# Performance work log

Hardware: AMD Instinct MI355X
Metric: run time of the kernel (lower is better)

Reference implementation:

```python
import jax, jax.numpy as jnp
import numpy as np

N = 100000        # nodes per batch
B = 1             # batch_size
E = 3200000       # edges
IN_F = 128        # in_features
ATT = 128         # attention_dim
HEADS = 8
DK = ATT // HEADS
SLOPE = 0.2       # leaky_relu_slope


def setup_inputs() -> dict:
    key = jax.random.key(0)
    k1, k2, k3, k4 = jax.random.split(key, 4)
    x = jax.random.normal(k1, (B * N, IN_F), dtype=jnp.float32)
    edge = jax.random.randint(k2, (B, 2, E), 0, N)
    # xavier_normal with gain=1.414 on W:[IN_F, ATT]
    W = jax.random.normal(k3, (IN_F, ATT), dtype=jnp.float32) * (1.414 * np.sqrt(2.0 / (IN_F + ATT)))
    # a originally [1, 2*d_k, 1, 1]; flattened to [2*d_k] (same math)
    a = jax.random.normal(k4, (2 * DK,), dtype=jnp.float32) * (1.414 * np.sqrt(2.0 / (2 * DK + 1)))
    return {"x": x, "edge": edge, "W": W, "a": a}


def _segment_softmax(scores, seg):
    # scores: [E, H], seg: [E] -> softmax within each segment (node id)
    smax = jax.ops.segment_max(scores, seg, num_segments=N)
    ex = jnp.exp(scores - smax[seg])
    denom = jax.ops.segment_sum(ex, seg, num_segments=N)
    return ex / denom[seg]


def reference(x, edge, W, a):
    wx = x @ W                                           # [B*N, ATT]
    h = wx.reshape(B, N, HEADS, DK).transpose(0, 1, 3, 2)  # [B, N, DK, H]
    a1, a2 = a[:DK], a[DK:]
    # sum(a * concat(h_src, h_dst)) = a1.h_src + a2.h_dst (linearity)
    s_src = jnp.einsum('bnkh,k->bnh', h, a1)             # [B, N, H]
    s_dst = jnp.einsum('bnkh,k->bnh', h, a2)             # [B, N, H]
    src = edge[:, 0, :]                                  # [B, E]
    dst = edge[:, 1, :]                                  # [B, E]
    gather = jax.vmap(lambda s, i: s[i])
    scores = gather(s_src, src) + gather(s_dst, dst)     # [B, E, H]
    edge_e = jnp.where(scores > 0, scores, SLOPE * scores)  # leaky relu
    # attention_norm_idx = 0 -> normalize over edges sharing a source node
    attention = jax.vmap(_segment_softmax)(edge_e, src)  # [B, E, H]
    return attention, wx
```

## Files before the change

kernel.cpp:

```cpp
#include <hip/hip_runtime.h>

#define N_NODES 100000
#define E_EDGES 3200000
#define IN_F 128
#define ATT 128
#define HEADS 8
#define DK 16
#define SLOPE 0.2f
#define NH (N_NODES * HEADS)

#define CHUNK 448
#define NBINS 224
#define NS 8
#define HB 512
#define EPB 6272

__global__ __launch_bounds__(256) void gemm_s_kernel(
    const float* __restrict__ x, const float* __restrict__ W,
    const float* __restrict__ a, float* __restrict__ wx,
    float* __restrict__ s_src, float* __restrict__ s_dst)
{
    __shared__ float xs[8][128];
    __shared__ float Ws[8][128];

    const int tid = threadIdx.x;
    const int ty  = tid >> 4;
    const int tx  = tid & 15;
    const int row0 = blockIdx.x * 128;

    float acc[8][8];
#pragma unroll
    for (int i = 0; i < 8; i++)
#pragma unroll
        for (int j = 0; j < 8; j++) acc[i][j] = 0.f;

    const int lrow  = tid >> 1;
    const int khalf = (tid & 1) * 4;
    const int wkk   = tid >> 5;
    const int wc    = (tid & 31) * 4;

    for (int k0 = 0; k0 < IN_F; k0 += 8) {
        float4 xv = make_float4(0.f, 0.f, 0.f, 0.f);
        const int grow = row0 + lrow;
        if (grow < N_NODES)
            xv = *(const float4*)(x + (size_t)grow * IN_F + k0 + khalf);
        const float4 wv = *(const float4*)(W + (size_t)(k0 + wkk) * ATT + wc);

        __syncthreads();
        xs[khalf + 0][lrow] = xv.x;
        xs[khalf + 1][lrow] = xv.y;
        xs[khalf + 2][lrow] = xv.z;
        xs[khalf + 3][lrow] = xv.w;
        *(float4*)(&Ws[wkk][wc]) = wv;
        __syncthreads();

#pragma unroll
        for (int kk = 0; kk < 8; kk++) {
            float av[8], bv[8];
            *(float4*)(av)     = *(const float4*)(&xs[kk][ty * 8]);
            *(float4*)(av + 4) = *(const float4*)(&xs[kk][ty * 8 + 4]);
            *(float4*)(bv)     = *(const float4*)(&Ws[kk][tx * 8]);
            *(float4*)(bv + 4) = *(const float4*)(&Ws[kk][tx * 8 + 4]);
#pragma unroll
            for (int r = 0; r < 8; r++)
#pragma unroll
                for (int c = 0; c < 8; c++)
                    acc[r][c] = fmaf(av[r], bv[c], acc[r][c]);
        }
    }

    const int koff = (tx & 1) * 8;
    const int head = tx >> 1;
    float a1[8], a2[8];
#pragma unroll
    for (int c = 0; c < 8; c++) {
        a1[c] = a[koff + c];
        a2[c] = a[DK + koff + c];
    }

#pragma unroll
    for (int r = 0; r < 8; r++) {
        const int grow = row0 + ty * 8 + r;
        const bool ok = (grow < N_NODES);
        if (ok) {
            *(float4*)(wx + (size_t)grow * ATT + tx * 8) =
                make_float4(acc[r][0], acc[r][1], acc[r][2], acc[r][3]);
            *(float4*)(wx + (size_t)grow * ATT + tx * 8 + 4) =
                make_float4(acc[r][4], acc[r][5], acc[r][6], acc[r][7]);
        }
        float p1 = 0.f, p2 = 0.f;
#pragma unroll
        for (int c = 0; c < 8; c++) {
            p1 = fmaf(acc[r][c], a1[c], p1);
            p2 = fmaf(acc[r][c], a2[c], p2);
        }
        p1 += __shfl_xor(p1, 1);
        p2 += __shfl_xor(p2, 1);
        if (((tx & 1) == 0) && ok) {
            s_src[(size_t)grow * HEADS + head] = p1;
            s_dst[(size_t)grow * HEADS + head] = p2;
        }
    }
}

__global__ __launch_bounds__(256) void hist_kernel(
    const int* __restrict__ src, int* __restrict__ counts)
{
    __shared__ int h[NBINS];
    const int t = threadIdx.x;
    const int b = blockIdx.x;
    for (int i = t; i < NBINS; i += 256) h[i] = 0;
    __syncthreads();

    const int rb = b * EPB;
    const int re = min(rb + EPB, E_EDGES);
    for (int i = rb + t * 4; i < re; i += 256 * 4) {
        const int4 s4 = *(const int4*)(src + i);
        atomicAdd(&h[s4.x / CHUNK], 1);
        atomicAdd(&h[s4.y / CHUNK], 1);
        atomicAdd(&h[s4.z / CHUNK], 1);
        atomicAdd(&h[s4.w / CHUNK], 1);
    }
    __syncthreads();
    for (int i = t; i < NBINS; i += 256) counts[i * HB + b] = h[i];
}

__global__ __launch_bounds__(1024) void scan_kernel(
    const int* __restrict__ counts, int* __restrict__ offs)
{
    __shared__ int part[1024];
    const int t = threadIdx.x;
    const int per = (NBINS * HB) / 1024;
    const int base = t * per;

    int sum = 0;
    for (int i = 0; i < per; i++) sum += counts[base + i];
    part[t] = sum;
    __syncthreads();

    for (int off = 1; off < 1024; off <<= 1) {
        int v = 0;
        if (t >= off) v = part[t - off];
        __syncthreads();
        if (t >= off) part[t] += v;
        __syncthreads();
    }

    int run = (t == 0) ? 0 : part[t - 1];
    for (int i = 0; i < per; i++) {
        offs[base + i] = run;
        run += counts[base + i];
    }
}

__global__ __launch_bounds__(256) void scatter_kernel(
    const int* __restrict__ src, const int* __restrict__ dst,
    const int* __restrict__ offs, unsigned int* __restrict__ binned)
{
    __shared__ int cur[NBINS];
    const int t = threadIdx.x;
    const int b = blockIdx.x;
    for (int i = t; i < NBINS; i += 256) cur[i] = offs[i * HB + b];
    __syncthreads();

    const int rb = b * EPB;
    const int re = min(rb + EPB, E_EDGES);
    for (int i = rb + t * 4; i < re; i += 256 * 4) {
        const int4 s4 = *(const int4*)(src + i);
        const int4 d4 = *(const int4*)(dst + i);
        const int ss[4] = {s4.x, s4.y, s4.z, s4.w};
        const int dd[4] = {d4.x, d4.y, d4.z, d4.w};
#pragma unroll
        for (int j = 0; j < 4; j++) {
            const int c = ss[j] / CHUNK;
            const int pos = atomicAdd(&cur[c], 1);
            binned[pos] = ((unsigned int)(ss[j] - c * CHUNK) << 17) |
                          (unsigned int)dd[j];
        }
    }
}

__global__ __launch_bounds__(256, 8) void denom_binned_kernel(
    const unsigned int* __restrict__ binned, const int* __restrict__ offs,
    const float* __restrict__ s_src, const float* __restrict__ s_dst,
    float* __restrict__ denoms)
{
    __shared__ float acc[HEADS][CHUNK + 1];

    const int t  = threadIdx.x;
    const int c  = blockIdx.x;
    const int j  = blockIdx.y;
    const int lo = c * CHUNK;
    const int hi = min(lo + CHUNK, N_NODES);

    for (int i = t; i < HEADS * (CHUNK + 1); i += 256)
        ((float*)acc)[i] = 0.f;
    __syncthreads();

    const int start = offs[c * HB];
    const int end   = (c + 1 < NBINS) ? offs[(c + 1) * HB] : E_EDGES;
    const int len   = end - start;
    const int e0 = start + (int)((long long)len * j / NS);
    const int e1 = start + (int)((long long)len * (j + 1) / NS);

    int i = e0 + t;
    bool v0 = i < e1;
    bool v1 = i + 256 < e1;
    unsigned int pw0 = v0 ? binned[i] : 0u;
    unsigned int pw1 = v1 ? binned[i + 256] : 0u;

    while (v0) {
        const unsigned int w0 = pw0;
        const unsigned int w1 = v1 ? pw1 : pw0;
        const bool cv1 = v1;

        i += 512;
        v0 = i < e1;
        v1 = i + 256 < e1;
        if (v0) pw0 = binned[i];
        if (v1) pw1 = binned[i + 256];

        const int di0 = w0 & 0x1FFFF, sl0 = w0 >> 17;
        const int di1 = w1 & 0x1FFFF, sl1 = w1 >> 17;
        const float4* ps0 = (const float4*)(s_src + (size_t)(lo + sl0) * HEADS);
        const float4* pd0 = (const float4*)(s_dst + (size_t)di0 * HEADS);
        const float4* ps1 = (const float4*)(s_src + (size_t)(lo + sl1) * HEADS);
        const float4* pd1 = (const float4*)(s_dst + (size_t)di1 * HEADS);
        const float4 xa0 = ps0[0], xa1 = ps0[1], xb0 = pd0[0], xb1 = pd0[1];
        const float4 ya0 = ps1[0], ya1 = ps1[1], yb0 = pd1[0], yb1 = pd1[1];
        const float s0[8] = {xa0.x + xb0.x, xa0.y + xb0.y, xa0.z + xb0.z, xa0.w + xb0.w,
                             xa1.x + xb1.x, xa1.y + xb1.y, xa1.z + xb1.z, xa1.w + xb1.w};
        const float s1[8] = {ya0.x + yb0.x, ya0.y + yb0.y, ya0.z + yb0.z, ya0.w + yb0.w,
                             ya1.x + yb1.x, ya1.y + yb1.y, ya1.z + yb1.z, ya1.w + yb1.w};
#pragma unroll
        for (int h = 0; h < 8; h++) {
            float v = s0[h]; v = v > 0.f ? v : SLOPE * v;
            atomicAdd(&acc[h][sl0], __expf(v));
        }
        if (cv1) {
#pragma unroll
            for (int h = 0; h < 8; h++) {
                float v = s1[h]; v = v > 0.f ? v : SLOPE * v;
                atomicAdd(&acc[h][sl1], __expf(v));
            }
        }
    }
    __syncthreads();

    float* outp = denoms + (size_t)j * NH + (size_t)lo * HEADS;
    for (int nd = t; nd < hi - lo; nd += 256) {
        const float4 o0 = make_float4(acc[0][nd], acc[1][nd], acc[2][nd], acc[3][nd]);
        const float4 o1 = make_float4(acc[4][nd], acc[5][nd], acc[6][nd], acc[7][nd]);
        *(float4*)(outp + (size_t)nd * 8)     = o0;
        *(float4*)(outp + (size_t)nd * 8 + 4) = o1;
    }
}

__global__ __launch_bounds__(256) void reduce_recip_kernel(float* __restrict__ denoms)
{
    const int i = blockIdx.x * 256 + threadIdx.x;
    if (i >= NH) return;
    float s = 0.f;
#pragma unroll
    for (int c = 0; c < NS; c++) s += denoms[(size_t)c * NH + i];
    denoms[i] = __frcp_rn(s);
}

__global__ __launch_bounds__(256) void norm_kernel(
    const int* __restrict__ src, const int* __restrict__ dst,
    const float* __restrict__ s_src, const float* __restrict__ s_dst,
    const float* __restrict__ rdenom, float* __restrict__ att)
{
    const int e = blockIdx.x * 256 + threadIdx.x;
    if (e >= E_EDGES) return;
    const int s = src[e];
    const int d = dst[e];
    const float4* ps = (const float4*)(s_src + (size_t)s * HEADS);
    const float4* pd = (const float4*)(s_dst + (size_t)d * HEADS);
    const float4 s0 = ps[0], s1 = ps[1], d0 = pd[0], d1 = pd[1];
    const float4* pr = (const float4*)(rdenom + (size_t)s * HEADS);
    const float4 r0 = pr[0], r1 = pr[1];
    float sc[8] = {s0.x + d0.x, s0.y + d0.y, s0.z + d0.z, s0.w + d0.w,
                   s1.x + d1.x, s1.y + d1.y, s1.z + d1.z, s1.w + d1.w};
    float rd[8] = {r0.x, r0.y, r0.z, r0.w, r1.x, r1.y, r1.z, r1.w};
    float o[8];
#pragma unroll
    for (int h = 0; h < 8; h++) {
        float v = sc[h];
        v = v > 0.f ? v : SLOPE * v;
        o[h] = __expf(v) * rd[h];
    }
    float4* po = (float4*)(att + (size_t)e * HEADS);
    po[0] = make_float4(o[0], o[1], o[2], o[3]);
    po[1] = make_float4(o[4], o[5], o[6], o[7]);
}

extern "C" void kernel_launch(void* const* d_in, const int* in_sizes, int n_in,
                              void* d_out, int out_size, void* d_ws, size_t ws_size,
                              hipStream_t stream)
{
    const float* x    = (const float*)d_in[0];
    const int*   edge = (const int*)d_in[1];
    const float* W    = (const float*)d_in[2];
    const float* a    = (const float*)d_in[3];

    float* out = (float*)d_out;
    float* att = out;
    float* wx  = out + (size_t)E_EDGES * HEADS;

    float* ws     = (float*)d_ws;
    float* s_src  = ws;
    float* s_dst  = s_src + (size_t)NH;
    float* denoms = s_dst + (size_t)NH;
    int*   counts = (int*)(denoms + (size_t)NS * NH);
    int*   offs   = counts + (size_t)NBINS * HB;

    unsigned int* binned = (unsigned int*)att;

    const int* src = edge;
    const int* dst = edge + E_EDGES;

    const int gemm_blocks = (N_NODES + 127) / 128;
    gemm_s_kernel<<<gemm_blocks, 256, 0, stream>>>(x, W, a, wx, s_src, s_dst);

    hist_kernel<<<HB, 256, 0, stream>>>(src, counts);
    scan_kernel<<<1, 1024, 0, stream>>>(counts, offs);
    scatter_kernel<<<HB, 256, 0, stream>>>(src, dst, offs, binned);

    dim3 bgrid(NBINS, NS);
    denom_binned_kernel<<<bgrid, 256, 0, stream>>>(binned, offs, s_src, s_dst, denoms);

    const int nblocks = (NH + 255) / 256;
    reduce_recip_kernel<<<nblocks, 256, 0, stream>>>(denoms);

    const int eblocks = (E_EDGES + 255) / 256;
    norm_kernel<<<eblocks, 256, 0, stream>>>(src, dst, s_src, s_dst, denoms, att);
}
```

Before: 557.1 us.

## Write unnormalized exp scores during binned denom pass, normalize in place

The binned denominator kernel now also carries the original edge index, computes the exp scores once, and scatters them directly into the attention output. The final pass only rescales by the reciprocal denominator, so it no longer gathers s_src and s_dst. The per-slice denominator buffers and the reduce kernel are replaced by global float atomics into one zeroed buffer. The source scores for each chunk are staged in shared memory. In exchange, the binned entries double to 8 bytes and move into workspace, att writes become scattered, the kernel allows fewer blocks per CU (launch bound 5 instead of 8), and denominator summation order is no longer deterministic.

```diff
diff --git a/kernel.cpp b/kernel.cpp
--- a/kernel.cpp
+++ b/kernel.cpp
@@ -103,6 +103,12 @@
     }
 }
 
+__global__ __launch_bounds__(256) void zero_kernel(float4* __restrict__ p)
+{
+    const int i = blockIdx.x * 256 + threadIdx.x;
+    if (i < NH / 4) p[i] = make_float4(0.f, 0.f, 0.f, 0.f);
+}
+
 __global__ __launch_bounds__(256) void hist_kernel(
     const int* __restrict__ src, int* __restrict__ counts)
 {
@@ -155,7 +161,7 @@
 
 __global__ __launch_bounds__(256) void scatter_kernel(
     const int* __restrict__ src, const int* __restrict__ dst,
-    const int* __restrict__ offs, unsigned int* __restrict__ binned)
+    const int* __restrict__ offs, uint2* __restrict__ binned)
 {
     __shared__ int cur[NBINS];
     const int t = threadIdx.x;
@@ -174,18 +180,20 @@
         for (int j = 0; j < 4; j++) {
             const int c = ss[j] / CHUNK;
             const int pos = atomicAdd(&cur[c], 1);
-            binned[pos] = ((unsigned int)(ss[j] - c * CHUNK) << 17) |
-                          (unsigned int)dd[j];
-        }
-    }
-}
-
-__global__ __launch_bounds__(256, 8) void denom_binned_kernel(
-    const unsigned int* __restrict__ binned, const int* __restrict__ offs,
+            binned[pos] = make_uint2(
+                ((unsigned int)(ss[j] - c * CHUNK) << 17) | (unsigned int)dd[j],
+                (unsigned int)(i + j));
+        }
+    }
+}
+
+__global__ __launch_bounds__(256, 5) void denom_binned_kernel(
+    const uint2* __restrict__ binned, const int* __restrict__ offs,
     const float* __restrict__ s_src, const float* __restrict__ s_dst,
-    float* __restrict__ denoms)
+    float* __restrict__ denoms, float* __restrict__ att)
 {
     __shared__ float acc[HEADS][CHUNK + 1];
+    __shared__ float ssrc[CHUNK * HEADS];
 
     const int t  = threadIdx.x;
     const int c  = blockIdx.x;
@@ -195,6 +203,12 @@
 
     for (int i = t; i < HEADS * (CHUNK + 1); i += 256)
         ((float*)acc)[i] = 0.f;
+    {
+        const int nf4 = (hi - lo) * 2;
+        const float4* sp = (const float4*)(s_src + (size_t)lo * HEADS);
+        float4* dp = (float4*)ssrc;
+        for (int i = t; i < nf4; i += 256) dp[i] = sp[i];
+    }
     __syncthreads();
 
     const int start = offs[c * HB];
@@ -206,12 +220,12 @@
     int i = e0 + t;
     bool v0 = i < e1;
     bool v1 = i + 256 < e1;
-    unsigned int pw0 = v0 ? binned[i] : 0u;
-    unsigned int pw1 = v1 ? binned[i + 256] : 0u;
+    uint2 pw0 = v0 ? binned[i] : make_uint2(0u, 0u);
+    uint2 pw1 = v1 ? binned[i + 256] : make_uint2(0u, 0u);
 
     while (v0) {
-        const unsigned int w0 = pw0;
-        const unsigned int w1 = v1 ? pw1 : pw0;
+        const uint2 w0 = pw0;
+        const uint2 w1 = v1 ? pw1 : pw0;
         const bool cv1 = v1;
 
         i += 512;
@@ -220,79 +234,79 @@
         if (v0) pw0 = binned[i];
         if (v1) pw1 = binned[i + 256];
 
-        const int di0 = w0 & 0x1FFFF, sl0 = w0 >> 17;
-        const int di1 = w1 & 0x1FFFF, sl1 = w1 >> 17;
-        const float4* ps0 = (const float4*)(s_src + (size_t)(lo + sl0) * HEADS);
+        const int sl0 = (int)(w0.x >> 17), di0 = (int)(w0.x & 0x1FFFFu);
+        const int sl1 = (int)(w1.x >> 17), di1 = (int)(w1.x & 0x1FFFFu);
+        const int ei0 = (int)w0.y, ei1 = (int)w1.y;
+
         const float4* pd0 = (const float4*)(s_dst + (size_t)di0 * HEADS);
-        const float4* ps1 = (const float4*)(s_src + (size_t)(lo + sl1) * HEADS);
         const float4* pd1 = (const float4*)(s_dst + (size_t)di1 * HEADS);
-        const float4 xa0 = ps0[0], xa1 = ps0[1], xb0 = pd0[0], xb1 = pd0[1];
-        const float4 ya0 = ps1[0], ya1 = ps1[1], yb0 = pd1[0], yb1 = pd1[1];
+        const float4 xb0 = pd0[0], xb1 = pd0[1];
+        const float4 yb0 = pd1[0], yb1 = pd1[1];
+        const float4* qs0 = (const float4*)(ssrc + sl0 * HEADS);
+        const float4* qs1 = (const float4*)(ssrc + sl1 * HEADS);
+        const float4 xa0 = qs0[0], xa1 = qs0[1];
+        const float4 ya0 = qs1[0], ya1 = qs1[1];
+
         const float s0[8] = {xa0.x + xb0.x, xa0.y + xb0.y, xa0.z + xb0.z, xa0.w + xb0.w,
                              xa1.x + xb1.x, xa1.y + xb1.y, xa1.z + xb1.z, xa1.w + xb1.w};
         const float s1[8] = {ya0.x + yb0.x, ya0.y + yb0.y, ya0.z + yb0.z, ya0.w + yb0.w,
                              ya1.x + yb1.x, ya1.y + yb1.y, ya1.z + yb1.z, ya1.w + yb1.w};
+        float ex0[8], ex1[8];
 #pragma unroll
         for (int h = 0; h < 8; h++) {
             float v = s0[h]; v = v > 0.f ? v : SLOPE * v;
-            atomicAdd(&acc[h][sl0], __expf(v));
-        }
+            ex0[h] = __expf(v);
+            float u = s1[h]; u = u > 0.f ? u : SLOPE * u;
+            ex1[h] = __expf(u);
+        }
+        {
+            float4* pa = (float4*)(att + (size_t)ei0 * HEADS);
+            pa[0] = make_float4(ex0[0], ex0[1], ex0[2], ex0[3]);
+            pa[1] = make_float4(ex0[4], ex0[5], ex0[6], ex0[7]);
+        }
+#pragma unroll
+        for (int h = 0; h < 8; h++)
+            atomicAdd(&acc[h][sl0], ex0[h]);
         if (cv1) {
-#pragma unroll
-            for (int h = 0; h < 8; h++) {
-                float v = s1[h]; v = v > 0.f ? v : SLOPE * v;
-                atomicAdd(&acc[h][sl1], __expf(v));
-            }
-        }
-    }
-    __syncthreads();
-
-    float* outp = denoms + (size_t)j * NH + (size_t)lo * HEADS;
+            float4* pa = (float4*)(att + (size_t)ei1 * HEADS);
+            pa[0] = make_float4(ex1[0], ex1[1], ex1[2], ex1[3]);
+            pa[1] = make_float4(ex1[4], ex1[5], ex1[6], ex1[7]);
+#pragma unroll
+            for (int h = 0; h < 8; h++)
+                atomicAdd(&acc[h][sl1], ex1[h]);
+        }
+    }
+    __syncthreads();
+
     for (int nd = t; nd < hi - lo; nd += 256) {
-        const float4 o0 = make_float4(acc[0][nd], acc[1][nd], acc[2][nd], acc[3][nd]);
-        const float4 o1 = make_float4(acc[4][nd], acc[5][nd], acc[6][nd], acc[7][nd]);
-        *(float4*)(outp + (size_t)nd * 8)     = o0;
-        *(float4*)(outp + (size_t)nd * 8 + 4) = o1;
-    }
-}
-
-__global__ __launch_bounds__(256) void reduce_recip_kernel(float* __restrict__ denoms)
-{
-    const int i = blockIdx.x * 256 + threadIdx.x;
-    if (i >= NH) return;
-    float s = 0.f;
-#pragma unroll
-    for (int c = 0; c < NS; c++) s += denoms[(size_t)c * NH + i];
-    denoms[i] = __frcp_rn(s);
+#pragma unroll
+        for (int h = 0; h < 8; h++)
+            unsafeAtomicAdd(&denoms[(size_t)(lo + nd) * HEADS + h], acc[h][nd]);
+    }
 }
 
 __global__ __launch_bounds__(256) void norm_kernel(
-    const int* __restrict__ src, const int* __restrict__ dst,
-    const float* __restrict__ s_src, const float* __restrict__ s_dst,
-    const float* __restrict__ rdenom, float* __restrict__ att)
+    const int* __restrict__ src, const float* __restrict__ denoms,
+    float* __restrict__ att)
 {
     const int e = blockIdx.x * 256 + threadIdx.x;
     if (e >= E_EDGES) return;
+    float4* pa = (float4*)(att + (size_t)e * HEADS);
+    const float4 x0 = pa[0], x1 = pa[1];
     const int s = src[e];
-    const int d = dst[e];
-    const float4* ps = (const float4*)(s_src + (size_t)s * HEADS);
-    const float4* pd = (const float4*)(s_dst + (size_t)d * HEADS);
-    const float4 s0 = ps[0], s1 = ps[1], d0 = pd[0], d1 = pd[1];
-    const float4* pr = (const float4*)(rdenom + (size_t)s * HEADS);
-    const float4 r0 = pr[0], r1 = pr[1];
-    float sc[8] = {s0.x + d0.x, s0.y + d0.y, s0.z + d0.z, s0.w + d0.w,
-                   s1.x + d1.x, s1.y + d1.y, s1.z + d1.z, s1.w + d1.w};
-    float rd[8] = {r0.x, r0.y, r0.z, r0.w, r1.x, r1.y, r1.z, r1.w};
-    float o[8];
-#pragma unroll
-    for (int h = 0; h < 8; h++) {
-        float v = sc[h];
-        v = v > 0.f ? v : SLOPE * v;
-        o[h] = __expf(v) * rd[h];
-    }
-    float4* po = (float4*)(att + (size_t)e * HEADS);
-    po[0] = make_float4(o[0], o[1], o[2], o[3]);
-    po[1] = make_float4(o[4], o[5], o[6], o[7]);
+    const float4* pd = (const float4*)(denoms + (size_t)s * HEADS);
+    const float4 d0 = pd[0], d1 = pd[1];
+    float4 o0, o1;
+    o0.x = x0.x * __frcp_rn(d0.x);
+    o0.y = x0.y * __frcp_rn(d0.y);
+    o0.z = x0.z * __frcp_rn(d0.z);
+    o0.w = x0.w * __frcp_rn(d0.w);
+    o1.x = x1.x * __frcp_rn(d1.x);
+    o1.y = x1.y * __frcp_rn(d1.y);
+    o1.z = x1.z * __frcp_rn(d1.z);
+    o1.w = x1.w * __frcp_rn(d1.w);
+    pa[0] = o0;
+    pa[1] = o1;
 }
 
 extern "C" void kernel_launch(void* const* d_in, const int* in_sizes, int n_in,
@@ -312,27 +326,25 @@
     float* s_src  = ws;
     float* s_dst  = s_src + (size_t)NH;
     float* denoms = s_dst + (size_t)NH;
-    int*   counts = (int*)(denoms + (size_t)NS * NH);
+    int*   counts = (int*)(denoms + (size_t)NH);
     int*   offs   = counts + (size_t)NBINS * HB;
-
-    unsigned int* binned = (unsigned int*)att;
+    uint2* binned = (uint2*)(offs + (size_t)NBINS * HB);
 
     const int* src = edge;
     const int* dst = edge + E_EDGES;
 
     const int gemm_blocks = (N_NODES + 127) / 128;
     gemm_s_kernel<<<gemm_blocks, 256, 0, stream>>>(x, W, a, wx, s_src, s_dst);
+
+    zero_kernel<<<(NH / 4 + 255) / 256, 256, 0, stream>>>((float4*)denoms);
 
     hist_kernel<<<HB, 256, 0, stream>>>(src, counts);
     scan_kernel<<<1, 1024, 0, stream>>>(counts, offs);
     scatter_kernel<<<HB, 256, 0, stream>>>(src, dst, offs, binned);
 
     dim3 bgrid(NBINS, NS);
-    denom_binned_kernel<<<bgrid, 256, 0, stream>>>(binned, offs, s_src, s_dst, denoms);
-
-    const int nblocks = (NH + 255) / 256;
-    reduce_recip_kernel<<<nblocks, 256, 0, stream>>>(denoms);
+    denom_binned_kernel<<<bgrid, 256, 0, stream>>>(binned, offs, s_src, s_dst, denoms, att);
 
     const int eblocks = (E_EDGES + 255) / 256;
-    norm_kernel<<<eblocks, 256, 0, stream>>>(src, dst, s_src, s_dst, denoms, att);
-}
+    norm_kernel<<<eblocks, 256, 0, stream>>>(src, denoms, att);
+}
```

Measured after the change: 556.6 us. No clear change (-0.1%).

## Reuse binned edge order in norm pass with LDS-staged source scores

Applied to the files above, without the earlier changes.

The scatter pass now stores each binned edge as a pair of packed (local src, dst) and original edge index, in workspace rather than aliased over the output. The normalization pass becomes a binned kernel that stages s_src and reciprocal denominators for the chunk in LDS and writes attention to the original edge position with nontemporal stores. The denominator pass also reads s_src from LDS, and both binned kernels use nontemporal 64-bit loads. This cuts random global gathers for source-side data, at the cost of doubled binned traffic, scattered output writes, and lower occupancy.

```diff
diff --git a/kernel.cpp b/kernel.cpp
--- a/kernel.cpp
+++ b/kernel.cpp
@@ -15,6 +15,20 @@
 #define HB 512
 #define EPB 6272
 
+typedef float vf4 __attribute__((ext_vector_type(4)));
+
+static __device__ __forceinline__ void nt_store4(float* p, float a, float b,
+                                                 float c, float d)
+{
+    vf4 v; v.x = a; v.y = b; v.z = c; v.w = d;
+    __builtin_nontemporal_store(v, (vf4*)p);
+}
+
+static __device__ __forceinline__ unsigned long long nt_load_u64(const void* p)
+{
+    return __builtin_nontemporal_load((const unsigned long long*)p);
+}
+
 __global__ __launch_bounds__(256) void gemm_s_kernel(
     const float* __restrict__ x, const float* __restrict__ W,
     const float* __restrict__ a, float* __restrict__ wx,
@@ -155,7 +169,7 @@
 
 __global__ __launch_bounds__(256) void scatter_kernel(
     const int* __restrict__ src, const int* __restrict__ dst,
-    const int* __restrict__ offs, unsigned int* __restrict__ binned)
+    const int* __restrict__ offs, uint2* __restrict__ binned)
 {
     __shared__ int cur[NBINS];
     const int t = threadIdx.x;
@@ -174,18 +188,20 @@
         for (int j = 0; j < 4; j++) {
             const int c = ss[j] / CHUNK;
             const int pos = atomicAdd(&cur[c], 1);
-            binned[pos] = ((unsigned int)(ss[j] - c * CHUNK) << 17) |
-                          (unsigned int)dd[j];
-        }
-    }
-}
-
-__global__ __launch_bounds__(256, 8) void denom_binned_kernel(
-    const unsigned int* __restrict__ binned, const int* __restrict__ offs,
+            binned[pos] = make_uint2(
+                ((unsigned int)(ss[j] - c * CHUNK) << 17) | (unsigned int)dd[j],
+                (unsigned int)(i + j));
+        }
+    }
+}
+
+__global__ __launch_bounds__(256, 5) void denom_binned_kernel(
+    const uint2* __restrict__ binned, const int* __restrict__ offs,
     const float* __restrict__ s_src, const float* __restrict__ s_dst,
     float* __restrict__ denoms)
 {
     __shared__ float acc[HEADS][CHUNK + 1];
+    __shared__ float ssrc[CHUNK * HEADS];
 
     const int t  = threadIdx.x;
     const int c  = blockIdx.x;
@@ -195,6 +211,12 @@
 
     for (int i = t; i < HEADS * (CHUNK + 1); i += 256)
         ((float*)acc)[i] = 0.f;
+    {
+        const int nf4 = (hi - lo) * 2;
+        const float4* sp = (const float4*)(s_src + (size_t)lo * HEADS);
+        float4* dp = (float4*)ssrc;
+        for (int i = t; i < nf4; i += 256) dp[i] = sp[i];
+    }
     __syncthreads();
 
     const int start = offs[c * HB];
@@ -206,28 +228,34 @@
     int i = e0 + t;
     bool v0 = i < e1;
     bool v1 = i + 256 < e1;
-    unsigned int pw0 = v0 ? binned[i] : 0u;
-    unsigned int pw1 = v1 ? binned[i + 256] : 0u;
+    unsigned long long pw0 = v0 ? nt_load_u64(binned + i) : 0ull;
+    unsigned long long pw1 = v1 ? nt_load_u64(binned + i + 256) : 0ull;
 
     while (v0) {
-        const unsigned int w0 = pw0;
-        const unsigned int w1 = v1 ? pw1 : pw0;
+        const unsigned long long w0 = pw0;
+        const unsigned long long w1 = v1 ? pw1 : pw0;
         const bool cv1 = v1;
 
         i += 512;
         v0 = i < e1;
         v1 = i + 256 < e1;
-        if (v0) pw0 = binned[i];
-        if (v1) pw1 = binned[i + 256];
-
-        const int di0 = w0 & 0x1FFFF, sl0 = w0 >> 17;
-        const int di1 = w1 & 0x1FFFF, sl1 = w1 >> 17;
-        const float4* ps0 = (const float4*)(s_src + (size_t)(lo + sl0) * HEADS);
+        if (v0) pw0 = nt_load_u64(binned + i);
+        if (v1) pw1 = nt_load_u64(binned + i + 256);
+
+        const unsigned int k0 = (unsigned int)w0;
+        const unsigned int k1 = (unsigned int)w1;
+        const int sl0 = (int)(k0 >> 17), di0 = (int)(k0 & 0x1FFFFu);
+        const int sl1 = (int)(k1 >> 17), di1 = (int)(k1 & 0x1FFFFu);
+
         const float4* pd0 = (const float4*)(s_dst + (size_t)di0 * HEADS);
-        const float4* ps1 = (const float4*)(s_src + (size_t)(lo + sl1) * HEADS);
         const float4* pd1 = (const float4*)(s_dst + (size_t)di1 * HEADS);
-        const float4 xa0 = ps0[0], xa1 = ps0[1], xb0 = pd0[0], xb1 = pd0[1];
-        const float4 ya0 = ps1[0], ya1 = ps1[1], yb0 = pd1[0], yb1 = pd1[1];
+        const float4 xb0 = pd0[0], xb1 = pd0[1];
+        const float4 yb0 = pd1[0], yb1 = pd1[1];
+        const float4* qs0 = (const float4*)(ssrc + sl0 * HEADS);
+        const float4* qs1 = (const float4*)(ssrc + sl1 * HEADS);
+        const float4 xa0 = qs0[0], xa1 = qs0[1];
+        const float4 ya0 = qs1[0], ya1 = qs1[1];
+
         const float s0[8] = {xa0.x + xb0.x, xa0.y + xb0.y, xa0.z + xb0.z, xa0.w + xb0.w,
                              xa1.x + xb1.x, xa1.y + xb1.y, xa1.z + xb1.z, xa1.w + xb1.w};
         const float s1[8] = {ya0.x + yb0.x, ya0.y + yb0.y, ya0.z + yb0.z, ya0.w + yb0.w,
@@ -266,33 +294,102 @@
     denoms[i] = __frcp_rn(s);
 }
 
-__global__ __launch_bounds__(256) void norm_kernel(
-    const int* __restrict__ src, const int* __restrict__ dst,
+__global__ __launch_bounds__(256, 5) void norm_binned_kernel(
+    const uint2* __restrict__ binned, const int* __restrict__ offs,
     const float* __restrict__ s_src, const float* __restrict__ s_dst,
     const float* __restrict__ rdenom, float* __restrict__ att)
 {
-    const int e = blockIdx.x * 256 + threadIdx.x;
-    if (e >= E_EDGES) return;
-    const int s = src[e];
-    const int d = dst[e];
-    const float4* ps = (const float4*)(s_src + (size_t)s * HEADS);
-    const float4* pd = (const float4*)(s_dst + (size_t)d * HEADS);
-    const float4 s0 = ps[0], s1 = ps[1], d0 = pd[0], d1 = pd[1];
-    const float4* pr = (const float4*)(rdenom + (size_t)s * HEADS);
-    const float4 r0 = pr[0], r1 = pr[1];
-    float sc[8] = {s0.x + d0.x, s0.y + d0.y, s0.z + d0.z, s0.w + d0.w,
-                   s1.x + d1.x, s1.y + d1.y, s1.z + d1.z, s1.w + d1.w};
-    float rd[8] = {r0.x, r0.y, r0.z, r0.w, r1.x, r1.y, r1.z, r1.w};
-    float o[8];
-#pragma unroll
-    for (int h = 0; h < 8; h++) {
-        float v = sc[h];
-        v = v > 0.f ? v : SLOPE * v;
-        o[h] = __expf(v) * rd[h];
-    }
-    float4* po = (float4*)(att + (size_t)e * HEADS);
-    po[0] = make_float4(o[0], o[1], o[2], o[3]);
-    po[1] = make_float4(o[4], o[5], o[6], o[7]);
+    __shared__ float ssrc[CHUNK * HEADS];
+    __shared__ float srd [CHUNK * HEADS];
+
+    const int t  = threadIdx.x;
+    const int c  = blockIdx.x;
+    const int j  = blockIdx.y;
+    const int lo = c * CHUNK;
+    const int hi = min(lo + CHUNK, N_NODES);
+
+    {
+        const int nf4 = (hi - lo) * 2;
+        const float4* sp = (const float4*)(s_src + (size_t)lo * HEADS);
+        const float4* rp = (const float4*)(rdenom + (size_t)lo * HEADS);
+        float4* dp = (float4*)ssrc;
+        float4* dr = (float4*)srd;
+        for (int i = t; i < nf4; i += 256) { dp[i] = sp[i]; dr[i] = rp[i]; }
+    }
+    __syncthreads();
+
+    const int start = offs[c * HB];
+    const int end   = (c + 1 < NBINS) ? offs[(c + 1) * HB] : E_EDGES;
+    const int len   = end - start;
+    const int e0 = start + (int)((long long)len * j / NS);
+    const int e1 = start + (int)((long long)len * (j + 1) / NS);
+
+    int i = e0 + t;
+    bool v0 = i < e1;
+    bool v1 = i + 256 < e1;
+    unsigned long long pw0 = v0 ? nt_load_u64(binned + i) : 0ull;
+    unsigned long long pw1 = v1 ? nt_load_u64(binned + i + 256) : 0ull;
+
+    while (v0) {
+        const unsigned long long w0 = pw0;
+        const unsigned long long w1 = v1 ? pw1 : pw0;
+        const bool cv1 = v1;
+
+        i += 512;
+        v0 = i < e1;
+        v1 = i + 256 < e1;
+        if (v0) pw0 = nt_load_u64(binned + i);
+        if (v1) pw1 = nt_load_u64(binned + i + 256);
+
+        const unsigned int k0 = (unsigned int)w0;
+        const unsigned int k1 = (unsigned int)w1;
+        const int sl0 = (int)(k0 >> 17), di0 = (int)(k0 & 0x1FFFFu);
+        const int sl1 = (int)(k1 >> 17), di1 = (int)(k1 & 0x1FFFFu);
+        const int ei0 = (int)(unsigned int)(w0 >> 32);
+        const int ei1 = (int)(unsigned int)(w1 >> 32);
+
+        const float4* pd0 = (const float4*)(s_dst + (size_t)di0 * HEADS);
+        const float4* pd1 = (const float4*)(s_dst + (size_t)di1 * HEADS);
+        const float4 xb0 = pd0[0], xb1 = pd0[1];
+        const float4 yb0 = pd1[0], yb1 = pd1[1];
+        const float4* qs0 = (const float4*)(ssrc + sl0 * HEADS);
+        const float4* qs1 = (const float4*)(ssrc + sl1 * HEADS);
+        const float4 xa0 = qs0[0], xa1 = qs0[1];
+        const float4 ya0 = qs1[0], ya1 = qs1[1];
+        const float4* qr0 = (const float4*)(srd + sl0 * HEADS);
+        const float4* qr1 = (const float4*)(srd + sl1 * HEADS);
+        const float4 xr0 = qr0[0], xr1 = qr0[1];
+        const float4 yr0 = qr1[0], yr1 = qr1[1];
+
+        const float s0[8] = {xa0.x + xb0.x, xa0.y + xb0.y, xa0.z + xb0.z, xa0.w + xb0.w,
+                             xa1.x + xb1.x, xa1.y + xb1.y, xa1.z + xb1.z, xa1.w + xb1.w};
+        const float r0[8] = {xr0.x, xr0.y, xr0.z, xr0.w, xr1.x, xr1.y, xr1.z, xr1.w};
+        float o0[8];
+#pragma unroll
+        for (int h = 0; h < 8; h++) {
+            float v = s0[h]; v = v > 0.f ? v : SLOPE * v;
+            o0[h] = __expf(v) * r0[h];
+        }
+        {
+            float* pa = att + (size_t)ei0 * HEADS;
+            nt_store4(pa,     o0[0], o0[1], o0[2], o0[3]);
+            nt_store4(pa + 4, o0[4], o0[5], o0[6], o0[7]);
+        }
+        if (cv1) {
+            const float s1[8] = {ya0.x + yb0.x, ya0.y + yb0.y, ya0.z + yb0.z, ya0.w + yb0.w,
+                                 ya1.x + yb1.x, ya1.y + yb1.y, ya1.z + yb1.z, ya1.w + yb1.w};
+            const float r1[8] = {yr0.x, yr0.y, yr0.z, yr0.w, yr1.x, yr1.y, yr1.z, yr1.w};
+            float o1[8];
+#pragma unroll
+            for (int h = 0; h < 8; h++) {
+                float v = s1[h]; v = v > 0.f ? v : SLOPE * v;
+                o1[h] = __expf(v) * r1[h];
+            }
+            float* pa = att + (size_t)ei1 * HEADS;
+            nt_store4(pa,     o1[0], o1[1], o1[2], o1[3]);
+            nt_store4(pa + 4, o1[4], o1[5], o1[6], o1[7]);
+        }
+    }
 }
 
 extern "C" void kernel_launch(void* const* d_in, const int* in_sizes, int n_in,
@@ -314,8 +411,7 @@
     float* denoms = s_dst + (size_t)NH;
     int*   counts = (int*)(denoms + (size_t)NS * NH);
     int*   offs   = counts + (size_t)NBINS * HB;
-
-    unsigned int* binned = (unsigned int*)att;
+    uint2* binned = (uint2*)(offs + (size_t)NBINS * HB);
 
     const int* src = edge;
     const int* dst = edge + E_EDGES;
@@ -333,6 +429,6 @@
     const int nblocks = (NH + 255) / 256;
     reduce_recip_kernel<<<nblocks, 256, 0, stream>>>(denoms);
 
-    const int eblocks = (E_EDGES + 255) / 256;
-    norm_kernel<<<eblocks, 256, 0, stream>>>(src, dst, s_src, s_dst, denoms, att);
-}
+    norm_binned_kernel<<<bgrid, 256, 0, stream>>>(binned, offs, s_src, s_dst,
+                                                  denoms, att);
+}
```

Measured after the change: 666.8 us. 19.7% more time.

## Interleave source scores with reciprocal denominators and stage source scores in LDS

Applied to the files above, without the earlier changes.

The GEMM now also writes s_src into an interleaved per-node buffer P whose second half holds the reciprocal softmax denominators written by the reduce kernel. The normalization kernel then fetches both from one 64-byte line per source and handles two edges per thread. The denominator kernel copies its chunk's s_src into shared memory rather than gathering it from global memory, and its occupancy hint is lowered to fit the larger LDS footprint. The binned buffer moves from aliasing the output to the workspace, which needs more workspace memory.

```diff
diff --git a/kernel.cpp b/kernel.cpp
--- a/kernel.cpp
+++ b/kernel.cpp
@@ -18,7 +18,8 @@
 __global__ __launch_bounds__(256) void gemm_s_kernel(
     const float* __restrict__ x, const float* __restrict__ W,
     const float* __restrict__ a, float* __restrict__ wx,
-    float* __restrict__ s_src, float* __restrict__ s_dst)
+    float* __restrict__ s_src, float* __restrict__ s_dst,
+    float* __restrict__ P)
 {
     __shared__ float xs[8][128];
     __shared__ float Ws[8][128];
@@ -99,6 +100,7 @@
         if (((tx & 1) == 0) && ok) {
             s_src[(size_t)grow * HEADS + head] = p1;
             s_dst[(size_t)grow * HEADS + head] = p2;
+            P[(size_t)grow * 16 + head] = p1;
         }
     }
 }
@@ -180,12 +182,13 @@
     }
 }
 
-__global__ __launch_bounds__(256, 8) void denom_binned_kernel(
+__global__ __launch_bounds__(256, 5) void denom_binned_kernel(
     const unsigned int* __restrict__ binned, const int* __restrict__ offs,
     const float* __restrict__ s_src, const float* __restrict__ s_dst,
     float* __restrict__ denoms)
 {
     __shared__ float acc[HEADS][CHUNK + 1];
+    __shared__ float ssrc[CHUNK * HEADS];
 
     const int t  = threadIdx.x;
     const int c  = blockIdx.x;
@@ -195,6 +198,12 @@
 
     for (int i = t; i < HEADS * (CHUNK + 1); i += 256)
         ((float*)acc)[i] = 0.f;
+    {
+        const int nf4 = (hi - lo) * 2;
+        const float4* sp = (const float4*)(s_src + (size_t)lo * HEADS);
+        float4* dp = (float4*)ssrc;
+        for (int i = t; i < nf4; i += 256) dp[i] = sp[i];
+    }
     __syncthreads();
 
     const int start = offs[c * HB];
@@ -220,14 +229,18 @@
         if (v0) pw0 = binned[i];
         if (v1) pw1 = binned[i + 256];
 
-        const int di0 = w0 & 0x1FFFF, sl0 = w0 >> 17;
-        const int di1 = w1 & 0x1FFFF, sl1 = w1 >> 17;
-        const float4* ps0 = (const float4*)(s_src + (size_t)(lo + sl0) * HEADS);
+        const int sl0 = (int)(w0 >> 17), di0 = (int)(w0 & 0x1FFFFu);
+        const int sl1 = (int)(w1 >> 17), di1 = (int)(w1 & 0x1FFFFu);
+
         const float4* pd0 = (const float4*)(s_dst + (size_t)di0 * HEADS);
-        const float4* ps1 = (const float4*)(s_src + (size_t)(lo + sl1) * HEADS);
         const float4* pd1 = (const float4*)(s_dst + (size_t)di1 * HEADS);
-        const float4 xa0 = ps0[0], xa1 = ps0[1], xb0 = pd0[0], xb1 = pd0[1];
-        const float4 ya0 = ps1[0], ya1 = ps1[1], yb0 = pd1[0], yb1 = pd1[1];
+        const float4 xb0 = pd0[0], xb1 = pd0[1];
+        const float4 yb0 = pd1[0], yb1 = pd1[1];
+        const float4* qs0 = (const float4*)(ssrc + sl0 * HEADS);
+        const float4* qs1 = (const float4*)(ssrc + sl1 * HEADS);
+        const float4 xa0 = qs0[0], xa1 = qs0[1];
+        const float4 ya0 = qs1[0], ya1 = qs1[1];
+
         const float s0[8] = {xa0.x + xb0.x, xa0.y + xb0.y, xa0.z + xb0.z, xa0.w + xb0.w,
                              xa1.x + xb1.x, xa1.y + xb1.y, xa1.z + xb1.z, xa1.w + xb1.w};
         const float s1[8] = {ya0.x + yb0.x, ya0.y + yb0.y, ya0.z + yb0.z, ya0.w + yb0.w,
@@ -256,43 +269,57 @@
     }
 }
 
-__global__ __launch_bounds__(256) void reduce_recip_kernel(float* __restrict__ denoms)
+__global__ __launch_bounds__(256) void reduce_recip_kernel(
+    const float* __restrict__ denoms, float* __restrict__ P)
 {
     const int i = blockIdx.x * 256 + threadIdx.x;
     if (i >= NH) return;
     float s = 0.f;
 #pragma unroll
     for (int c = 0; c < NS; c++) s += denoms[(size_t)c * NH + i];
-    denoms[i] = __frcp_rn(s);
-}
-
-__global__ __launch_bounds__(256) void norm_kernel(
+    P[(size_t)(i >> 3) * 16 + 8 + (i & 7)] = __frcp_rn(s);
+}
+
+__global__ __launch_bounds__(256) void norm_e_kernel(
     const int* __restrict__ src, const int* __restrict__ dst,
-    const float* __restrict__ s_src, const float* __restrict__ s_dst,
-    const float* __restrict__ rdenom, float* __restrict__ att)
-{
-    const int e = blockIdx.x * 256 + threadIdx.x;
-    if (e >= E_EDGES) return;
-    const int s = src[e];
-    const int d = dst[e];
-    const float4* ps = (const float4*)(s_src + (size_t)s * HEADS);
-    const float4* pd = (const float4*)(s_dst + (size_t)d * HEADS);
-    const float4 s0 = ps[0], s1 = ps[1], d0 = pd[0], d1 = pd[1];
-    const float4* pr = (const float4*)(rdenom + (size_t)s * HEADS);
-    const float4 r0 = pr[0], r1 = pr[1];
-    float sc[8] = {s0.x + d0.x, s0.y + d0.y, s0.z + d0.z, s0.w + d0.w,
-                   s1.x + d1.x, s1.y + d1.y, s1.z + d1.z, s1.w + d1.w};
-    float rd[8] = {r0.x, r0.y, r0.z, r0.w, r1.x, r1.y, r1.z, r1.w};
-    float o[8];
+    const float* __restrict__ P, const float* __restrict__ s_dst,
+    float* __restrict__ att)
+{
+    const int e0 = (blockIdx.x * 256 + threadIdx.x) * 2;
+    if (e0 >= E_EDGES) return;
+    const int2 sp = *(const int2*)(src + e0);
+    const int2 dp = *(const int2*)(dst + e0);
+
+    const float4* p0 = (const float4*)(P + (size_t)sp.x * 16);
+    const float4* p1 = (const float4*)(P + (size_t)sp.y * 16);
+    const float4* q0 = (const float4*)(s_dst + (size_t)dp.x * HEADS);
+    const float4* q1 = (const float4*)(s_dst + (size_t)dp.y * HEADS);
+    const float4 sa0 = p0[0], sa1 = p0[1], ra0 = p0[2], ra1 = p0[3];
+    const float4 sb0 = p1[0], sb1 = p1[1], rb0 = p1[2], rb1 = p1[3];
+    const float4 da0 = q0[0], da1 = q0[1];
+    const float4 db0 = q1[0], db1 = q1[1];
+
+    const float s0[8] = {sa0.x + da0.x, sa0.y + da0.y, sa0.z + da0.z, sa0.w + da0.w,
+                         sa1.x + da1.x, sa1.y + da1.y, sa1.z + da1.z, sa1.w + da1.w};
+    const float r0[8] = {ra0.x, ra0.y, ra0.z, ra0.w, ra1.x, ra1.y, ra1.z, ra1.w};
+    const float s1[8] = {sb0.x + db0.x, sb0.y + db0.y, sb0.z + db0.z, sb0.w + db0.w,
+                         sb1.x + db1.x, sb1.y + db1.y, sb1.z + db1.z, sb1.w + db1.w};
+    const float r1[8] = {rb0.x, rb0.y, rb0.z, rb0.w, rb1.x, rb1.y, rb1.z, rb1.w};
+
+    float o0[8], o1[8];
 #pragma unroll
     for (int h = 0; h < 8; h++) {
-        float v = sc[h];
-        v = v > 0.f ? v : SLOPE * v;
-        o[h] = __expf(v) * rd[h];
-    }
-    float4* po = (float4*)(att + (size_t)e * HEADS);
-    po[0] = make_float4(o[0], o[1], o[2], o[3]);
-    po[1] = make_float4(o[4], o[5], o[6], o[7]);
+        float v = s0[h]; v = v > 0.f ? v : SLOPE * v;
+        o0[h] = __expf(v) * r0[h];
+        float u = s1[h]; u = u > 0.f ? u : SLOPE * u;
+        o1[h] = __expf(u) * r1[h];
+    }
+
+    float4* pa = (float4*)(att + (size_t)e0 * HEADS);
+    pa[0] = make_float4(o0[0], o0[1], o0[2], o0[3]);
+    pa[1] = make_float4(o0[4], o0[5], o0[6], o0[7]);
+    pa[2] = make_float4(o1[0], o1[1], o1[2], o1[3]);
+    pa[3] = make_float4(o1[4], o1[5], o1[6], o1[7]);
 }
 
 extern "C" void kernel_launch(void* const* d_in, const int* in_sizes, int n_in,
@@ -311,17 +338,17 @@
     float* ws     = (float*)d_ws;
     float* s_src  = ws;
     float* s_dst  = s_src + (size_t)NH;
-    float* denoms = s_dst + (size_t)NH;
+    float* P      = s_dst + (size_t)NH;
+    float* denoms = P + (size_t)2 * NH;
     int*   counts = (int*)(denoms + (size_t)NS * NH);
     int*   offs   = counts + (size_t)NBINS * HB;
-
-    unsigned int* binned = (unsigned int*)att;
+    unsigned int* binned = (unsigned int*)(offs + (size_t)NBINS * HB);
 
     const int* src = edge;
     const int* dst = edge + E_EDGES;
 
     const int gemm_blocks = (N_NODES + 127) / 128;
-    gemm_s_kernel<<<gemm_blocks, 256, 0, stream>>>(x, W, a, wx, s_src, s_dst);
+    gemm_s_kernel<<<gemm_blocks, 256, 0, stream>>>(x, W, a, wx, s_src, s_dst, P);
 
     hist_kernel<<<HB, 256, 0, stream>>>(src, counts);
     scan_kernel<<<1, 1024, 0, stream>>>(counts, offs);
@@ -331,8 +358,8 @@
     denom_binned_kernel<<<bgrid, 256, 0, stream>>>(binned, offs, s_src, s_dst, denoms);
 
     const int nblocks = (NH + 255) / 256;
-    reduce_recip_kernel<<<nblocks, 256, 0, stream>>>(denoms);
-
-    const int eblocks = (E_EDGES + 255) / 256;
-    norm_kernel<<<eblocks, 256, 0, stream>>>(src, dst, s_src, s_dst, denoms, att);
-}
+    reduce_recip_kernel<<<nblocks, 256, 0, stream>>>(denoms, P);
+
+    const int eblocks = (E_EDGES / 2 + 255) / 256;
+    norm_e_kernel<<<eblocks, 256, 0, stream>>>(src, dst, P, s_dst, att);
+}
```

Measured after the change: 550.9 us. No clear change (-1.1%).
